# Optimization experiments

Hardware: AMD Instinct MI355X
Metric: run time of the kernel (lower is better)

Reference implementation:

```python
import jax, jax.numpy as jnp
import numpy as np

MXFP_BLOCK = 32
FP32_MIN_NORMAL = 2.0 ** (-126)
# fp8_e4m3 element format params (bit_width=8)
EXP_BITS = 4
MBITS = 8            # mantissa bits incl. sign, used as 2**(MBITS-2) fixed-point scale
EMAX = 8
MAX_NORM = 448.0     # 2**8 * 1.75
SCALE_EMAX = 127.0   # 2**(MXFP_SCALE_BITS-1) - 1
MIN_PEXP = -6.0      # -2**(EXP_BITS-1) + 2


def _round_away(x):
    return jnp.sign(x) * jnp.floor(jnp.abs(x) + 0.5)


def mxfp_quant_lastdim(x):
    """Block-wise MXFP fp8_e4m3 fake quant along the last dim (block=32, no padding needed)."""
    shape = x.shape
    xb = x.reshape(shape[:-1] + (shape[-1] // MXFP_BLOCK, MXFP_BLOCK))
    shared = jnp.max(jnp.abs(xb), axis=-1, keepdims=True)
    zero_mask = (shared == 0).astype(xb.dtype)
    shared_exp = jnp.floor(jnp.log2(shared + FP32_MIN_NORMAL * zero_mask)) - EMAX
    shared_exp = jnp.where(shared_exp > SCALE_EMAX, jnp.nan, shared_exp)
    shared_exp = jnp.maximum(shared_exp, -SCALE_EMAX)
    scale = jnp.exp2(shared_exp)
    v = xb / scale
    # per-element private exponent, fixed-point mantissa rounding
    pexp = jnp.floor(jnp.log2(jnp.abs(v) + (v == 0).astype(v.dtype)))
    pexp = jnp.maximum(pexp, MIN_PEXP)
    pscale = jnp.exp2(pexp)
    m = 2.0 ** (MBITS - 2)  # 64
    q = _round_away(v / pscale * m) * pscale / m
    q = jnp.clip(q, -MAX_NORM, MAX_NORM)
    return (q * scale).reshape(shape)


def setup_inputs() -> dict:
    key = jax.random.key(0)
    k1, k2, k3 = jax.random.split(key, 3)
    B, S, DIN, DOUT = 8, 8192, 1024, 1024
    x = jax.random.normal(k1, (B, S, DIN), dtype=jnp.float32)
    weight = jax.random.normal(k2, (DOUT, DIN), dtype=jnp.float32) * 0.02
    bias = jax.random.normal(k3, (DOUT,), dtype=jnp.float32) * 0.02
    return {"x": x, "weight": weight, "bias": bias}


def reference(x, weight, bias):
    xq = mxfp_quant_lastdim(x)          # per-token blocks along features
    wq = mxfp_quant_lastdim(weight)     # per-output-channel blocks along in_features
    return jnp.einsum('bsd,od->bso', xq, wq) + bias
```

## Files before the change

kernel.cpp:

```cpp
#include <hip/hip_runtime.h>
#include <cstdint>
#include <cstddef>

#define MM 65536
#define NN 1024
#define KK 1024
#define NT 16

typedef __bf16 bf16x8 __attribute__((ext_vector_type(8)));
typedef float f32x4 __attribute__((ext_vector_type(4)));

typedef const __attribute__((address_space(1))) unsigned int* gas_t;
typedef __attribute__((address_space(3))) unsigned int* las_t;

__device__ __forceinline__ void gll16(const void* g, void* l) {
  __builtin_amdgcn_global_load_lds((gas_t)g, (las_t)l, 16, 0, 0);
}

__device__ __forceinline__ float exp2i(int e) {
  return __int_as_float((e + 127) << 23);
}

__device__ __forceinline__ f32x4 mfma(bf16x8 a, bf16x8 b, f32x4 c) {
  return __builtin_amdgcn_mfma_f32_16x16x32_bf16(a, b, c, 0, 0, 0);
}

__global__ __launch_bounds__(256) void mxfp_quant(const float* __restrict__ in,
                                                  unsigned short* __restrict__ out) {
  size_t i = (size_t)blockIdx.x * 256 + threadIdx.x;
  float4 v = ((const float4*)in)[i];
  float a = fmaxf(fmaxf(fabsf(v.x), fabsf(v.y)), fmaxf(fabsf(v.z), fabsf(v.w)));
  a = fmaxf(a, __shfl_xor(a, 1));
  a = fmaxf(a, __shfl_xor(a, 2));
  a = fmaxf(a, __shfl_xor(a, 4));
  int ebits = (int)((__float_as_uint(a) >> 23) & 0xff);
  int se = (ebits > 0 ? ebits : 1) - 127 - 8;
  se = se < -126 ? -126 : se;
  float sinv = exp2i(-se);
  float sc = exp2i(se);

  float e[4] = {v.x, v.y, v.z, v.w};
  unsigned short o[4];
#pragma unroll
  for (int c = 0; c < 4; ++c) {
    float vv = e[c] * sinv;
    int pe = (int)((__float_as_uint(vv) >> 23) & 0xff) - 127;
    pe = pe < -6 ? -6 : pe;
    float r = floorf(fabsf(vv) * exp2i(6 - pe) + 0.5f);
    float q = copysignf(r * exp2i(pe - 6), vv);
    q = fminf(fmaxf(q, -448.f), 448.f);
    float res = q * sc;
    o[c] = (unsigned short)(__float_as_uint(res) >> 16);
  }
  ushort4 ov = {o[0], o[1], o[2], o[3]};
  ((ushort4*)out)[i] = ov;
}

__global__ __launch_bounds__(512, 2) void gemm_bt(const unsigned short* __restrict__ A,
                                                  const unsigned short* __restrict__ B,
                                                  const float* __restrict__ bias,
                                                  float* __restrict__ C) {
  __shared__ unsigned short As[2][256 * 64];
  __shared__ unsigned short Bs[2][256 * 64];
  const int t = threadIdx.x;
  const int wg = ((blockIdx.x & 7) << 7) | (blockIdx.x >> 3);
  const int m0 = (wg >> 2) << 8;
  const int n0 = (wg & 3) << 8;

  const int lane = t & 63, w = t >> 6;
  const int wm = (w >> 2) << 7;
  const int wn = (w & 3) << 6;
  const int quad = lane >> 4, r16 = lane & 15;

  const int rt = t >> 3;
  const int cl = (t & 7) ^ (rt & 7);
  const unsigned short* Ag = A + (size_t)(m0 + rt) * KK + cl * 8;
  const unsigned short* Bg = B + (size_t)(n0 + rt) * KK + cl * 8;
  char* AsW = (char*)As + t * 16;
  char* BsW = (char*)Bs + t * 16;
  const char* AsR = (const char*)As + (wm + r16) * 128;
  const char* BsR = (const char*)Bs + (wn + r16) * 128;
  const int sw0 = (quad ^ (r16 & 7)) << 4;
  const int sw1 = ((4 | quad) ^ (r16 & 7)) << 4;

#define STG_A(BUF, H, C_, T_)                                                     \
  gll16(Ag + (size_t)((H) * 128 + (C_) * 64) * KK + (size_t)(T_) * 64,            \
        AsW + (BUF) * 32768 + (H) * 16384 + (C_) * 8192)
#define STG_B(BUF, H, C_, T_)                                                     \
  gll16(Bg + (size_t)((H) * 128 + (C_) * 64) * KK + (size_t)(T_) * 64,            \
        BsW + (BUF) * 32768 + (H) * 16384 + (C_) * 8192)
#define LDA(BUF, MP, SW) (*(const bf16x8*)(AsR + (BUF) * 32768 + (MP) * 2048 + (SW)))
#define LDB(BUF, NP, SW) (*(const bf16x8*)(BsR + (BUF) * 32768 + (NP) * 2048 + (SW)))
#define MFMA16(MB)                                              \
  do {                                                          \
    acc[(MB) + 0][0] = mfma(a0, b0, acc[(MB) + 0][0]);          \
    acc[(MB) + 0][1] = mfma(a0, b1, acc[(MB) + 0][1]);          \
    acc[(MB) + 0][2] = mfma(a0, b2, acc[(MB) + 0][2]);          \
    acc[(MB) + 0][3] = mfma(a0, b3, acc[(MB) + 0][3]);          \
    acc[(MB) + 1][0] = mfma(a1, b0, acc[(MB) + 1][0]);          \
    acc[(MB) + 1][1] = mfma(a1, b1, acc[(MB) + 1][1]);          \
    acc[(MB) + 1][2] = mfma(a1, b2, acc[(MB) + 1][2]);          \
    acc[(MB) + 1][3] = mfma(a1, b3, acc[(MB) + 1][3]);          \
    acc[(MB) + 2][0] = mfma(a2, b0, acc[(MB) + 2][0]);          \
    acc[(MB) + 2][1] = mfma(a2, b1, acc[(MB) + 2][1]);          \
    acc[(MB) + 2][2] = mfma(a2, b2, acc[(MB) + 2][2]);          \
    acc[(MB) + 2][3] = mfma(a2, b3, acc[(MB) + 2][3]);          \
    acc[(MB) + 3][0] = mfma(a3, b0, acc[(MB) + 3][0]);          \
    acc[(MB) + 3][1] = mfma(a3, b1, acc[(MB) + 3][1]);          \
    acc[(MB) + 3][2] = mfma(a3, b2, acc[(MB) + 3][2]);          \
    acc[(MB) + 3][3] = mfma(a3, b3, acc[(MB) + 3][3]);          \
  } while (0)

  f32x4 acc[8][4] = {};

  STG_A(0, 0, 0, 0); STG_A(0, 0, 1, 0);
  STG_A(0, 1, 0, 0); STG_A(0, 1, 1, 0);
  STG_B(0, 0, 0, 0); STG_B(0, 0, 1, 0);
  STG_B(0, 1, 0, 0); STG_B(0, 1, 1, 0);

#pragma unroll 2
  for (int kt = 0; kt < NT; ++kt) {
    const int bi = kt & 1;
    const int nx = bi ^ 1;
    const bool pf = (kt + 1) < NT;
    bf16x8 a0, a1, a2, a3, b0, b1, b2, b3;

    if (pf) {
      STG_A(nx, 0, 0, kt + 1); STG_A(nx, 0, 1, kt + 1);
      asm volatile("s_waitcnt vmcnt(2)" ::: "memory");
    } else {
      asm volatile("s_waitcnt vmcnt(0)" ::: "memory");
    }
    __builtin_amdgcn_s_barrier();
    asm volatile("" ::: "memory");
    a0 = LDA(bi, 0, sw0); a1 = LDA(bi, 1, sw0); a2 = LDA(bi, 2, sw0); a3 = LDA(bi, 3, sw0);
    b0 = LDB(bi, 0, sw0); b1 = LDB(bi, 1, sw0); b2 = LDB(bi, 2, sw0); b3 = LDB(bi, 3, sw0);
    __builtin_amdgcn_s_setprio(1);
    MFMA16(0);
    __builtin_amdgcn_s_setprio(0);
    __builtin_amdgcn_s_barrier();

    a0 = LDA(bi, 4, sw0); a1 = LDA(bi, 5, sw0); a2 = LDA(bi, 6, sw0); a3 = LDA(bi, 7, sw0);
    if (pf) { STG_A(nx, 1, 0, kt + 1); STG_A(nx, 1, 1, kt + 1); }
    __builtin_amdgcn_s_barrier();
    __builtin_amdgcn_s_setprio(1);
    MFMA16(4);
    __builtin_amdgcn_s_setprio(0);
    __builtin_amdgcn_s_barrier();

    a0 = LDA(bi, 0, sw1); a1 = LDA(bi, 1, sw1); a2 = LDA(bi, 2, sw1); a3 = LDA(bi, 3, sw1);
    b0 = LDB(bi, 0, sw1); b1 = LDB(bi, 1, sw1); b2 = LDB(bi, 2, sw1); b3 = LDB(bi, 3, sw1);
    if (pf) { STG_B(nx, 0, 0, kt + 1); STG_B(nx, 0, 1, kt + 1); }
    __builtin_amdgcn_s_barrier();
    __builtin_amdgcn_s_setprio(1);
    MFMA16(0);
    __builtin_amdgcn_s_setprio(0);
    __builtin_amdgcn_s_barrier();

    a0 = LDA(bi, 4, sw1); a1 = LDA(bi, 5, sw1); a2 = LDA(bi, 6, sw1); a3 = LDA(bi, 7, sw1);
    if (pf) { STG_B(nx, 1, 0, kt + 1); STG_B(nx, 1, 1, kt + 1); }
    __builtin_amdgcn_s_barrier();
    __builtin_amdgcn_s_setprio(1);
    MFMA16(4);
    __builtin_amdgcn_s_setprio(0);
    __builtin_amdgcn_s_barrier();
  }

  float bcol[4];
#pragma unroll
  for (int j = 0; j < 4; ++j) bcol[j] = bias[n0 + wn + j * 16 + r16];
#pragma unroll
  for (int mp = 0; mp < 8; ++mp) {
    const int rbase = m0 + wm + mp * 16 + quad * 4;
#pragma unroll
    for (int j = 0; j < 4; ++j) {
      const int col = n0 + wn + j * 16 + r16;
      float* Cp = C + (size_t)rbase * NN + col;
#pragma unroll
      for (int reg = 0; reg < 4; ++reg)
        Cp[(size_t)reg * NN] = acc[mp][j][reg] + bcol[j];
    }
  }
#undef STG_A
#undef STG_B
#undef LDA
#undef LDB
#undef MFMA16
}

extern "C" void kernel_launch(void* const* d_in, const int* in_sizes, int n_in,
                              void* d_out, int out_size, void* d_ws, size_t ws_size,
                              hipStream_t stream) {
  const float* x = (const float*)d_in[0];
  const float* wgt = (const float*)d_in[1];
  const float* bias = (const float*)d_in[2];
  float* out = (float*)d_out;

  unsigned short* xq = (unsigned short*)d_ws;
  unsigned short* wq = xq + (size_t)MM * KK;

  mxfp_quant<<<(MM * (size_t)KK) / 1024, 256, 0, stream>>>(x, xq);
  mxfp_quant<<<(NN * (size_t)KK) / 1024, 256, 0, stream>>>(wgt, wq);
  gemm_bt<<<(MM / 256) * (NN / 256), 512, 0, stream>>>(xq, wq, bias, out);
}
```

Before: 594.1 us.

## Split LDS tiles into K-halves so the first half computes before the second lands

Reorganizes the shared-memory layout of A and B tiles into two 32-wide K halves with 64-byte rows and a new XOR swizzle, and changes the global-to-LDS load mapping to four threads per row. The prologue and loop now wait only for the first K-half (vmcnt 6/4) before starting MFMAs, then wait for the second half later, so loads overlap more with compute. The risk is a different LDS bank-conflict profile from the new swizzle, and a fragile vmcnt accounting that could read data before it arrives.

```diff
diff --git a/kernel.cpp b/kernel.cpp
--- a/kernel.cpp
+++ b/kernel.cpp
@@ -60,8 +60,8 @@
                                                   const unsigned short* __restrict__ B,
                                                   const float* __restrict__ bias,
                                                   float* __restrict__ C) {
-  __shared__ unsigned short As[2][256 * 64];
-  __shared__ unsigned short Bs[2][256 * 64];
+  __shared__ unsigned short As[2][2][128 * 64];
+  __shared__ unsigned short Bs[2][2][128 * 64];
   const int t = threadIdx.x;
   const int wg = ((blockIdx.x & 7) << 7) | (blockIdx.x >> 3);
   const int m0 = (wg >> 2) << 8;
@@ -72,25 +72,26 @@
   const int wn = (w & 3) << 6;
   const int quad = lane >> 4, r16 = lane & 15;
 
-  const int rt = t >> 3;
-  const int cl = (t & 7) ^ (rt & 7);
-  const unsigned short* Ag = A + (size_t)(m0 + rt) * KK + cl * 8;
-  const unsigned short* Bg = B + (size_t)(n0 + rt) * KK + cl * 8;
+  const int rt = t >> 2;
+  const int lc = (t & 3) ^ ((rt >> 1) & 3);
+  const unsigned short* Ag = A + (size_t)(m0 + rt) * KK + lc * 8;
+  const unsigned short* Bg = B + (size_t)(n0 + rt) * KK + lc * 8;
   char* AsW = (char*)As + t * 16;
   char* BsW = (char*)Bs + t * 16;
-  const char* AsR = (const char*)As + (wm + r16) * 128;
-  const char* BsR = (const char*)Bs + (wn + r16) * 128;
-  const int sw0 = (quad ^ (r16 & 7)) << 4;
-  const int sw1 = ((4 | quad) ^ (r16 & 7)) << 4;
-
-#define STG_A(BUF, H, C_, T_)                                                     \
-  gll16(Ag + (size_t)((H) * 128 + (C_) * 64) * KK + (size_t)(T_) * 64,            \
-        AsW + (BUF) * 32768 + (H) * 16384 + (C_) * 8192)
-#define STG_B(BUF, H, C_, T_)                                                     \
-  gll16(Bg + (size_t)((H) * 128 + (C_) * 64) * KK + (size_t)(T_) * 64,            \
-        BsW + (BUF) * 32768 + (H) * 16384 + (C_) * 8192)
-#define LDA(BUF, MP, SW) (*(const bf16x8*)(AsR + (BUF) * 32768 + (MP) * 2048 + (SW)))
-#define LDB(BUF, NP, SW) (*(const bf16x8*)(BsR + (BUF) * 32768 + (NP) * 2048 + (SW)))
+  const int swq = (quad ^ ((r16 >> 1) & 3)) << 4;
+  const char* AsR = (const char*)As + (wm + r16) * 64 + swq;
+  const char* BsR = (const char*)Bs + (wn + r16) * 64 + swq;
+
+#define STG_A(BUF, KH, H, T_)                                              \
+  gll16(Ag + (size_t)(H) * 128 * KK + (size_t)(T_) * 64 + (KH) * 32,       \
+        AsW + (BUF) * 32768 + (KH) * 16384 + (H) * 8192)
+#define STG_B(BUF, KH, H, T_)                                              \
+  gll16(Bg + (size_t)(H) * 128 * KK + (size_t)(T_) * 64 + (KH) * 32,       \
+        BsW + (BUF) * 32768 + (KH) * 16384 + (H) * 8192)
+#define LDA(BUF, KH, MP) \
+  (*(const bf16x8*)(AsR + (BUF) * 32768 + (KH) * 16384 + (MP) * 1024))
+#define LDB(BUF, KH, NP) \
+  (*(const bf16x8*)(BsR + (BUF) * 32768 + (KH) * 16384 + (NP) * 1024))
 #define MFMA16(MB)                                              \
   do {                                                          \
     acc[(MB) + 0][0] = mfma(a0, b0, acc[(MB) + 0][0]);          \
@@ -114,8 +115,8 @@
   f32x4 acc[8][4] = {};
 
   STG_A(0, 0, 0, 0); STG_A(0, 0, 1, 0);
+  STG_B(0, 0, 0, 0); STG_B(0, 0, 1, 0);
   STG_A(0, 1, 0, 0); STG_A(0, 1, 1, 0);
-  STG_B(0, 0, 0, 0); STG_B(0, 0, 1, 0);
   STG_B(0, 1, 0, 0); STG_B(0, 1, 1, 0);
 
 #pragma unroll 2
@@ -127,37 +128,43 @@
 
     if (pf) {
       STG_A(nx, 0, 0, kt + 1); STG_A(nx, 0, 1, kt + 1);
-      asm volatile("s_waitcnt vmcnt(2)" ::: "memory");
+      asm volatile("s_waitcnt vmcnt(6)" ::: "memory");
+    } else {
+      asm volatile("s_waitcnt vmcnt(4)" ::: "memory");
+    }
+    __builtin_amdgcn_s_barrier();
+    asm volatile("" ::: "memory");
+    a0 = LDA(bi, 0, 0); a1 = LDA(bi, 0, 1); a2 = LDA(bi, 0, 2); a3 = LDA(bi, 0, 3);
+    b0 = LDB(bi, 0, 0); b1 = LDB(bi, 0, 1); b2 = LDB(bi, 0, 2); b3 = LDB(bi, 0, 3);
+    __builtin_amdgcn_s_setprio(1);
+    MFMA16(0);
+    __builtin_amdgcn_s_setprio(0);
+    __builtin_amdgcn_s_barrier();
+
+    a0 = LDA(bi, 0, 4); a1 = LDA(bi, 0, 5); a2 = LDA(bi, 0, 6); a3 = LDA(bi, 0, 7);
+    if (pf) { STG_B(nx, 0, 0, kt + 1); STG_B(nx, 0, 1, kt + 1); }
+    __builtin_amdgcn_s_barrier();
+    __builtin_amdgcn_s_setprio(1);
+    MFMA16(4);
+    __builtin_amdgcn_s_setprio(0);
+    __builtin_amdgcn_s_barrier();
+
+    if (pf) {
+      STG_A(nx, 1, 0, kt + 1); STG_A(nx, 1, 1, kt + 1);
+      asm volatile("s_waitcnt vmcnt(6)" ::: "memory");
     } else {
       asm volatile("s_waitcnt vmcnt(0)" ::: "memory");
     }
     __builtin_amdgcn_s_barrier();
     asm volatile("" ::: "memory");
-    a0 = LDA(bi, 0, sw0); a1 = LDA(bi, 1, sw0); a2 = LDA(bi, 2, sw0); a3 = LDA(bi, 3, sw0);
-    b0 = LDB(bi, 0, sw0); b1 = LDB(bi, 1, sw0); b2 = LDB(bi, 2, sw0); b3 = LDB(bi, 3, sw0);
+    a0 = LDA(bi, 1, 0); a1 = LDA(bi, 1, 1); a2 = LDA(bi, 1, 2); a3 = LDA(bi, 1, 3);
+    b0 = LDB(bi, 1, 0); b1 = LDB(bi, 1, 1); b2 = LDB(bi, 1, 2); b3 = LDB(bi, 1, 3);
     __builtin_amdgcn_s_setprio(1);
     MFMA16(0);
     __builtin_amdgcn_s_setprio(0);
     __builtin_amdgcn_s_barrier();
 
-    a0 = LDA(bi, 4, sw0); a1 = LDA(bi, 5, sw0); a2 = LDA(bi, 6, sw0); a3 = LDA(bi, 7, sw0);
-    if (pf) { STG_A(nx, 1, 0, kt + 1); STG_A(nx, 1, 1, kt + 1); }
-    __builtin_amdgcn_s_barrier();
-    __builtin_amdgcn_s_setprio(1);
-    MFMA16(4);
-    __builtin_amdgcn_s_setprio(0);
-    __builtin_amdgcn_s_barrier();
-
-    a0 = LDA(bi, 0, sw1); a1 = LDA(bi, 1, sw1); a2 = LDA(bi, 2, sw1); a3 = LDA(bi, 3, sw1);
-    b0 = LDB(bi, 0, sw1); b1 = LDB(bi, 1, sw1); b2 = LDB(bi, 2, sw1); b3 = LDB(bi, 3, sw1);
-    if (pf) { STG_B(nx, 0, 0, kt + 1); STG_B(nx, 0, 1, kt + 1); }
-    __builtin_amdgcn_s_barrier();
-    __builtin_amdgcn_s_setprio(1);
-    MFMA16(0);
-    __builtin_amdgcn_s_setprio(0);
-    __builtin_amdgcn_s_barrier();
-
-    a0 = LDA(bi, 4, sw1); a1 = LDA(bi, 5, sw1); a2 = LDA(bi, 6, sw1); a3 = LDA(bi, 7, sw1);
+    a0 = LDA(bi, 1, 4); a1 = LDA(bi, 1, 5); a2 = LDA(bi, 1, 6); a3 = LDA(bi, 1, 7);
     if (pf) { STG_B(nx, 1, 0, kt + 1); STG_B(nx, 1, 1, kt + 1); }
     __builtin_amdgcn_s_barrier();
     __builtin_amdgcn_s_setprio(1);
```

Measured after the change: 580.0 us. -2.4%, faster.
